# Optimization experiments

Hardware: AMD Instinct MI355X
Metric: run time of the kernel (lower is better)

## Reference

```python
import jax, jax.numpy as jnp
import numpy as np

N_HEAD = 16

def setup_inputs() -> dict:
    key = jax.random.key(0)
    k1, k2, k3, k4, k5 = jax.random.split(key, 5)
    B, T, C = 8, 2048, 1024
    hs = C // N_HEAD  # 64
    return {
        "ids": jax.random.normal(k1, (B, T, C), dtype=jnp.float32),
        "qkv_w": jax.random.normal(k2, (3 * hs, C), dtype=jnp.float32) * (C ** -0.5),
        "qkv_b": jax.random.normal(k3, (3 * hs,), dtype=jnp.float32) * 0.02,
        "proj_w": jax.random.normal(k4, (C, C), dtype=jnp.float32) * (C ** -0.5),
        "proj_b": jax.random.normal(k5, (C,), dtype=jnp.float32) * 0.02,
    }

def reference(ids, qkv_w, qkv_b, proj_w, proj_b):
    B, T, C = ids.shape
    hs = qkv_w.shape[0] // 3  # head_size
    # All heads share the same qkv Linear (input is replicated per-head in the
    # original), so compute one head and tile at the end.
    qkv = ids @ qkv_w.T + qkv_b                      # [B,T,3*hs]
    q, k, v = jnp.split(qkv, 3, axis=-1)             # each [B,T,hs]
    wei = jnp.einsum('btd,bsd->bts', q, k)           # [B,T,T]
    tril = jnp.tril(jnp.ones((T, T), dtype=bool))
    wei = jnp.where(tril, wei, jnp.float32(0.0))     # causal mask (no softmax)
    out_h = jnp.einsum('bts,bsd->btd', wei, v)       # [B,T,hs]
    out = jnp.tile(out_h, (1, 1, N_HEAD))            # identical heads concatenated
    return out @ proj_w.T + proj_b                   # [B,T,C]
```

## Files before the change

### kernel.cpp

```cpp
#include <hip/hip_runtime.h>
#include <hip/hip_bf16.h>

#define Bsz 8
#define Tsz 2048
#define Csz 1024
#define HSsz 64
#define NQ 192

typedef __attribute__((ext_vector_type(8))) short short8v;
typedef __attribute__((ext_vector_type(4))) float f32x4;
typedef unsigned short ushortT;
typedef unsigned int uintT;

__device__ __forceinline__ unsigned int f2bf(float f) {
    union { float f; unsigned int u; } v; v.f = f;
    return (v.u + 0x7fffu + ((v.u >> 16) & 1u)) >> 16;
}

__device__ __forceinline__ unsigned int pk2bf(float lo, float hi) {
    union { __hip_bfloat162 h2; unsigned int u; } cv;
    cv.h2 = __float22bfloat162_rn(float2{lo, hi});
    return cv.u;
}

__device__ __forceinline__ void glds16(const float* g, float* l) {
    __builtin_amdgcn_global_load_lds(
        (const __attribute__((address_space(1))) unsigned int*)(g),
        (__attribute__((address_space(3))) unsigned int*)(l),
        16, 0, 0);
}

__global__ __launch_bounds__(256) void k_prep(const float* __restrict__ qw,
                                              const float* __restrict__ pw,
                                              ushortT* __restrict__ wB,
                                              ushortT* __restrict__ w2a) {
    const int blk = blockIdx.x;
    if (blk < 96) {
        int idx = blk * 256 + threadIdx.x;
        int l = idx & 63;
        int ksjt = idx >> 6;
        int jt = ksjt % 12, ks = ksjt / 12;
        int j = jt * 16 + (l & 15);
        int k = ks * 32 + (l >> 4) * 8;
        const float* src = &qw[j * Csz + k];
        float4 a = *(const float4*)src;
        float4 b = *(const float4*)(src + 4);
        uint4 o;
        o.x = f2bf(a.x) | (f2bf(a.y) << 16);
        o.y = f2bf(a.z) | (f2bf(a.w) << 16);
        o.z = f2bf(b.x) | (f2bf(b.y) << 16);
        o.w = f2bf(b.z) | (f2bf(b.w) << 16);
        *(uint4*)&wB[(size_t)idx * 8] = o;
    } else {
        int idx = (blk - 96) * 256 + threadIdx.x;
        int l = idx & 63;
        int rest = idx >> 6;
        int m = rest & 63, ks = rest >> 6;
        int c = m * 16 + (l & 15);
        int d0 = ks * 32 + (l >> 4) * 8;
        float s0 = 0, s1 = 0, s2 = 0, s3 = 0, s4 = 0, s5 = 0, s6 = 0, s7 = 0;
#pragma unroll
        for (int hh = 0; hh < 16; ++hh) {
            const float* p = &pw[c * Csz + hh * HSsz + d0];
            float4 x = *(const float4*)p;
            float4 y = *(const float4*)(p + 4);
            s0 += x.x; s1 += x.y; s2 += x.z; s3 += x.w;
            s4 += y.x; s5 += y.y; s6 += y.z; s7 += y.w;
        }
        uint4 o;
        o.x = f2bf(s0) | (f2bf(s1) << 16);
        o.y = f2bf(s2) | (f2bf(s3) << 16);
        o.z = f2bf(s4) | (f2bf(s5) << 16);
        o.w = f2bf(s6) | (f2bf(s7) << 16);
        *(uint4*)&w2a[(size_t)idx * 8] = o;
    }
}

__global__ __launch_bounds__(512, 4) void k_qkv_mfma(const float* __restrict__ ids,
                                                     const ushortT* __restrict__ wB,
                                                     const float* __restrict__ bias,
                                                     ushortT* __restrict__ Qf,
                                                     ushortT* __restrict__ Kf,
                                                     ushortT* __restrict__ Vf) {
    __shared__ float sAf[2][4096];
    uintT* Lqk = (uintT*)&sAf[0][0];
    uintT* Lv  = Lqk + 32 * 68;

    const int tid = threadIdx.x;
    const int wv  = tid >> 6;
    const int l   = tid & 63;
    const int wm  = wv >> 2;
    const int wn  = wv & 3;
    const int lg  = l >> 4, ll = l & 15;

    const int row0 = blockIdx.x * 32;

    const int r0 = 4 * wv + (l >> 5);
    const int r2 = r0 + 2;
    const int g  = l & 31;
    const float* s0 = ids + (size_t)(row0 + r0) * Csz + ((g ^ (r0 & 7)) << 2);
    const float* s1 = ids + (size_t)(row0 + r2) * Csz + ((g ^ (r2 & 7)) << 2);

    const int afrow = wm * 16 + ll;
    const int e = ll & 7;

    f32x4 acc[3];
    acc[0] = acc[1] = acc[2] = (f32x4){0.f, 0.f, 0.f, 0.f};

    const ushortT* bbase_p = wB + ((size_t)(wn * 3) * 64 + l) * 8;

    glds16(s0, &sAf[0][wv * 512]);
    glds16(s1, &sAf[0][wv * 512 + 256]);

    for (int c = 0; c < 8; ++c) {
        __syncthreads();
        if (c < 7) {
            glds16(s0 + (c + 1) * 128, &sAf[(c + 1) & 1][wv * 512]);
            glds16(s1 + (c + 1) * 128, &sAf[(c + 1) & 1][wv * 512 + 256]);
        }
        const float* bufp = &sAf[c & 1][0];
#pragma unroll
        for (int kk = 0; kk < 4; ++kk) {
            const ushortT* bp = bbase_p + (size_t)(4 * c + kk) * 6144;
            short8v b0 = *(const short8v*)(bp);
            short8v b1 = *(const short8v*)(bp + 512);
            short8v b2 = *(const short8v*)(bp + 1024);

            const int G0 = kk * 8 + lg * 2;
            float4 a0 = *(const float4*)&bufp[afrow * 128 + ((G0 ^ e) << 2)];
            float4 a1 = *(const float4*)&bufp[afrow * 128 + (((G0 + 1) ^ e) << 2)];

            union { short8v s; unsigned int u[4]; } af;
            af.u[0] = pk2bf(a0.x, a0.y); af.u[1] = pk2bf(a0.z, a0.w);
            af.u[2] = pk2bf(a1.x, a1.y); af.u[3] = pk2bf(a1.z, a1.w);

            acc[0] = __builtin_amdgcn_mfma_f32_16x16x32_bf16(af.s, b0, acc[0], 0, 0, 0);
            acc[1] = __builtin_amdgcn_mfma_f32_16x16x32_bf16(af.s, b1, acc[1], 0, 0, 0);
            acc[2] = __builtin_amdgcn_mfma_f32_16x16x32_bf16(af.s, b2, acc[2], 0, 0, 0);
        }
    }
    __syncthreads();

    const int crow_l = wm * 16 + lg * 4;
    ushortT* L16 = (ushortT*)Lqk;
#pragma unroll
    for (int n = 0; n < 3; ++n) {
        const int jb = wn * 3 + n;
        const int j  = jb * 16 + ll;
        const float bj = bias[j];
        float v0 = acc[n][0] + bj, v1 = acc[n][1] + bj;
        float v2 = acc[n][2] + bj, v3 = acc[n][3] + bj;
        if (jb < 8) {
            ushortT* p = &L16[crow_l * 136 + j];
            p[0]   = (ushortT)f2bf(v0);
            p[136] = (ushortT)f2bf(v1);
            p[272] = (ushortT)f2bf(v2);
            p[408] = (ushortT)f2bf(v3);
        } else {
            uintT* p = &Lv[(j - 128) * 20 + (crow_l >> 1)];
            p[0] = pk2bf(v0, v1);
            p[1] = pk2bf(v2, v3);
        }
    }
    __syncthreads();

    const int l2 = tid & 63, ll2 = l2 & 15, lg2 = l2 >> 4;
    if (tid < 256) {
        const int ks = (tid >> 6) & 1, m = tid >> 7;
        uint4 q = *(const uint4*)&Lqk[(m * 16 + ll2) * 68 + ks * 16 + lg2 * 4];
        *(uint4*)&Qf[(((size_t)(row0 >> 4) + m) * 2 + ks) * 512 + l2 * 8] = q;
        const int n = tid >> 6;
        uint4 v = *(const uint4*)&Lv[(n * 16 + ll2) * 20 + lg2 * 4];
        const int bb = row0 >> 11, s32 = (row0 >> 5) & 63;
        *(uint4*)&Vf[((((size_t)bb * 64 + s32) * 4 + n) * 64 + l2) * 8] = v;
    } else {
        const int ks = (tid >> 6) & 1, m = (tid >> 7) & 1;
        uint4 k = *(const uint4*)&Lqk[(m * 16 + ll2) * 68 + 32 + ks * 16 + lg2 * 4];
        *(uint4*)&Kf[(((size_t)(row0 >> 4) + m) * 2 + ks) * 512 + l2 * 8] = k;
    }
}

__global__ __launch_bounds__(256, 3) void k_attn_mfma(const ushortT* __restrict__ Qf,
                                                      const ushortT* __restrict__ Kf,
                                                      const ushortT* __restrict__ Vf,
                                                      ushortT* __restrict__ hf) {
    __shared__ uintT su[4 * 2 * 16 * 36];
    __shared__ float s_o[4][32 * 68];

    const int tid = threadIdx.x;
    const int w  = tid >> 6;
    const int l  = tid & 63;
    const int lg = l >> 4;
    const int ll = l & 15;

    const int u = blockIdx.x;
    const int b = u & 7;
    const int si = 63 - (u >> 3);

    const int nT  = (si >> 1) + 1;
    const int qn  = nT >> 2, rem = nT & 3;
    const int t0  = w * qn + (w < rem ? w : rem);
    const int cnt = qn + (w < rem ? 1 : 0);

    const int gq = b * 128 + si * 2;

    short8v qf[2][2];
#pragma unroll
    for (int mt = 0; mt < 2; ++mt)
#pragma unroll
        for (int ks = 0; ks < 2; ++ks)
            qf[mt][ks] = *(const short8v*)&Qf[(((size_t)gq + mt) * 2 + ks) * 512 + l * 8];

    f32x4 oacc[2][4];
#pragma unroll
    for (int mt = 0; mt < 2; ++mt)
#pragma unroll
        for (int n = 0; n < 4; ++n) oacc[mt][n] = (f32x4){0.f, 0.f, 0.f, 0.f};

    for (int tile = t0; tile < t0 + cnt; ++tile) {
        const int gs = b * 128 + tile * 4;
        short8v kf[4][2];
#pragma unroll
        for (int ms = 0; ms < 4; ++ms) {
            const ushortT* kp = &Kf[(((size_t)gs + ms) * 2) * 512 + l * 8];
            kf[ms][0] = *(const short8v*)kp;
            kf[ms][1] = *(const short8v*)(kp + 512);
        }
        f32x4 sacc[4][2];
#pragma unroll
        for (int ms = 0; ms < 4; ++ms)
#pragma unroll
            for (int mt = 0; mt < 2; ++mt) sacc[ms][mt] = (f32x4){0.f, 0.f, 0.f, 0.f};
#pragma unroll
        for (int ms = 0; ms < 4; ++ms)
#pragma unroll
            for (int mt = 0; mt < 2; ++mt) {
                sacc[ms][mt] = __builtin_amdgcn_mfma_f32_16x16x32_bf16(kf[ms][0], qf[mt][0], sacc[ms][mt], 0, 0, 0);
                sacc[ms][mt] = __builtin_amdgcn_mfma_f32_16x16x32_bf16(kf[ms][1], qf[mt][1], sacc[ms][mt], 0, 0, 0);
            }
        if (tile == nT - 1) {
#pragma unroll
            for (int ms = 0; ms < 4; ++ms)
#pragma unroll
                for (int mt = 0; mt < 2; ++mt) {
                    const int tg = si * 32 + mt * 16 + ll;
#pragma unroll
                    for (int rr2 = 0; rr2 < 4; ++rr2) {
                        int sg = tile * 64 + ms * 16 + 4 * lg + rr2;
                        if (sg > tg) sacc[ms][mt][rr2] = 0.f;
                    }
                }
        }
#pragma unroll
        for (int mt = 0; mt < 2; ++mt)
#pragma unroll
            for (int ms = 0; ms < 4; ++ms) {
                uint2 pk;
                pk.x = pk2bf(sacc[ms][mt][0], sacc[ms][mt][1]);
                pk.y = pk2bf(sacc[ms][mt][2], sacc[ms][mt][3]);
                *(uint2*)&su[((w * 2 + mt) * 16 + ll) * 36 + ms * 8 + 2 * lg] = pk;
            }
        union { uint4 u4; short8v s; } pa[2][2];
#pragma unroll
        for (int mt = 0; mt < 2; ++mt)
#pragma unroll
            for (int h = 0; h < 2; ++h)
                pa[mt][h].u4 = *(const uint4*)&su[((w * 2 + mt) * 16 + ll) * 36 + h * 16 + lg * 4];

        const int gv = b * 64 + tile * 2;
        short8v vf[2][4];
#pragma unroll
        for (int h = 0; h < 2; ++h)
#pragma unroll
            for (int n = 0; n < 4; ++n)
                vf[h][n] = *(const short8v*)&Vf[((((size_t)gv + h) * 4 + n) * 64 + l) * 8];
#pragma unroll
        for (int mt = 0; mt < 2; ++mt)
#pragma unroll
            for (int n = 0; n < 4; ++n) {
                oacc[mt][n] = __builtin_amdgcn_mfma_f32_16x16x32_bf16(pa[mt][0].s, vf[0][n], oacc[mt][n], 0, 0, 0);
                oacc[mt][n] = __builtin_amdgcn_mfma_f32_16x16x32_bf16(pa[mt][1].s, vf[1][n], oacc[mt][n], 0, 0, 0);
            }
    }

#pragma unroll
    for (int mt = 0; mt < 2; ++mt)
#pragma unroll
        for (int n = 0; n < 4; ++n)
#pragma unroll
            for (int rr2 = 0; rr2 < 4; ++rr2)
                s_o[w][(mt * 16 + 4 * lg + rr2) * 68 + 16 * n + ll] = oacc[mt][n][rr2];
    __syncthreads();

    const int l2 = tid & 63, ll2 = l2 & 15, lg2 = l2 >> 4;
    const int ks = (tid >> 6) & 1, mt = tid >> 7;
    const int t = mt * 16 + ll2, dd = ks * 32 + lg2 * 8;
    float4 A = {0, 0, 0, 0}, B2 = {0, 0, 0, 0};
#pragma unroll
    for (int w2 = 0; w2 < 4; ++w2) {
        const float4 x = *(const float4*)&s_o[w2][t * 68 + dd];
        const float4 y = *(const float4*)&s_o[w2][t * 68 + dd + 4];
        A.x += x.x; A.y += x.y; A.z += x.z; A.w += x.w;
        B2.x += y.x; B2.y += y.y; B2.z += y.z; B2.w += y.w;
    }
    uint4 o;
    o.x = pk2bf(A.x, A.y);  o.y = pk2bf(A.z, A.w);
    o.z = pk2bf(B2.x, B2.y); o.w = pk2bf(B2.z, B2.w);
    *(uint4*)&hf[(((size_t)(b * 128 + si * 2) + mt) * 2 + ks) * 512 + l2 * 8] = o;
}

__global__ __launch_bounds__(256) void k_proj_mfma(const ushortT* __restrict__ hf,
                                                   const ushortT* __restrict__ w2a,
                                                   const float* __restrict__ pb,
                                                   float* __restrict__ out) {
    const int tid = threadIdx.x;
    const int w = tid >> 6, l = tid & 63;
    const size_t M0 = (size_t)blockIdx.x * 2;

    short8v hA0 = *(const short8v*)&hf[(M0 * 2 + 0) * 512 + l * 8];
    short8v hA1 = *(const short8v*)&hf[(M0 * 2 + 1) * 512 + l * 8];
    short8v hB0 = *(const short8v*)&hf[((M0 + 1) * 2 + 0) * 512 + l * 8];
    short8v hB1 = *(const short8v*)&hf[((M0 + 1) * 2 + 1) * 512 + l * 8];

    const int row = (l >> 4) * 4;
    const int tcol = l & 15;
    const size_t outA = (M0 * 16 + tcol) * Csz;
    const size_t outB = ((M0 + 1) * 16 + tcol) * Csz;

#pragma unroll 2
    for (int m = w * 16; m < w * 16 + 16; ++m) {
        const ushortT* ap = w2a + (size_t)(m * 64 + l) * 8;
        short8v a0 = *(const short8v*)ap;
        short8v a1 = *(const short8v*)(ap + 32768);
        const int c0 = m * 16 + row;
        const float4 pv = *(const float4*)&pb[c0];

        f32x4 accA = (f32x4){0.f, 0.f, 0.f, 0.f};
        accA = __builtin_amdgcn_mfma_f32_16x16x32_bf16(a0, hA0, accA, 0, 0, 0);
        accA = __builtin_amdgcn_mfma_f32_16x16x32_bf16(a1, hA1, accA, 0, 0, 0);
        f32x4 accB = (f32x4){0.f, 0.f, 0.f, 0.f};
        accB = __builtin_amdgcn_mfma_f32_16x16x32_bf16(a0, hB0, accB, 0, 0, 0);
        accB = __builtin_amdgcn_mfma_f32_16x16x32_bf16(a1, hB1, accB, 0, 0, 0);

        float4 oA, oB;
        oA.x = accA[0] + pv.x; oA.y = accA[1] + pv.y;
        oA.z = accA[2] + pv.z; oA.w = accA[3] + pv.w;
        oB.x = accB[0] + pv.x; oB.y = accB[1] + pv.y;
        oB.z = accB[2] + pv.z; oB.w = accB[3] + pv.w;
        *(float4*)&out[outA + c0] = oA;
        *(float4*)&out[outB + c0] = oB;
    }
}

extern "C" void kernel_launch(void* const* d_in, const int* in_sizes, int n_in,
                              void* d_out, int out_size, void* d_ws, size_t ws_size,
                              hipStream_t stream) {
    const float* ids    = (const float*)d_in[0];
    const float* qkv_w  = (const float*)d_in[1];
    const float* qkv_b  = (const float*)d_in[2];
    const float* proj_w = (const float*)d_in[3];
    const float* proj_b = (const float*)d_in[4];
    float* out = (float*)d_out;

    ushortT* Qf  = (ushortT*)d_ws;
    ushortT* Kf  = Qf + 16384 * HSsz;
    ushortT* Vf  = Kf + 16384 * HSsz;
    ushortT* hf  = Vf + 16384 * HSsz;
    ushortT* wB  = hf + 16384 * HSsz;
    ushortT* w2a = wB + 196608;

    hipLaunchKernelGGL(k_prep,      dim3(128), dim3(256), 0, stream, qkv_w, proj_w, wB, w2a);
    hipLaunchKernelGGL(k_qkv_mfma,  dim3(512), dim3(512), 0, stream, ids, wB, qkv_b, Qf, Kf, Vf);
    hipLaunchKernelGGL(k_attn_mfma, dim3(512), dim3(256), 0, stream, Qf, Kf, Vf, hf);
    hipLaunchKernelGGL(k_proj_mfma, dim3(512), dim3(256), 0, stream, hf, w2a, proj_b, out);
}
```

Measured before the change: 59.95 us.

## Use linear-attention prefix K^T V sums to replace off-chunk attention tiles

Because there is no softmax, the causal product can be split by associativity. A new kernel computes prefix sums of K^T V per 256-row chunk (stored in bf16), and the attention kernel then handles only the at most 4 diagonal-chunk tiles directly, adding Q·M for everything earlier. This removes the quadratic off-diagonal QK^T/PV work. In exchange it adds an extra Ktf transpose write, an extra launch, a serial prefix loop in k_kvsum (64 blocks, up to 56 iterations), and bf16 rounding of the accumulated prefix matrix.

```diff
diff --git a/kernel.cpp b/kernel.cpp
--- a/kernel.cpp
+++ b/kernel.cpp
@@ -81,10 +81,12 @@
                                                      const float* __restrict__ bias,
                                                      ushortT* __restrict__ Qf,
                                                      ushortT* __restrict__ Kf,
-                                                     ushortT* __restrict__ Vf) {
+                                                     ushortT* __restrict__ Vf,
+                                                     ushortT* __restrict__ Ktf) {
     __shared__ float sAf[2][4096];
     uintT* Lqk = (uintT*)&sAf[0][0];
     uintT* Lv  = Lqk + 32 * 68;
+    uintT* Lkt = Lv + 64 * 20;
 
     const int tid = threadIdx.x;
     const int wv  = tid >> 6;
@@ -156,6 +158,11 @@
             p[136] = (ushortT)f2bf(v1);
             p[272] = (ushortT)f2bf(v2);
             p[408] = (ushortT)f2bf(v3);
+            if (jb >= 4) {
+                uintT* pk = &Lkt[(j - 64) * 20 + (crow_l >> 1)];
+                pk[0] = pk2bf(v0, v1);
+                pk[1] = pk2bf(v2, v3);
+            }
         } else {
             uintT* p = &Lv[(j - 128) * 20 + (crow_l >> 1)];
             p[0] = pk2bf(v0, v1);
@@ -165,24 +172,71 @@
     __syncthreads();
 
     const int l2 = tid & 63, ll2 = l2 & 15, lg2 = l2 >> 4;
+    const int bb = row0 >> 11, s32 = (row0 >> 5) & 63;
     if (tid < 256) {
         const int ks = (tid >> 6) & 1, m = tid >> 7;
         uint4 q = *(const uint4*)&Lqk[(m * 16 + ll2) * 68 + ks * 16 + lg2 * 4];
         *(uint4*)&Qf[(((size_t)(row0 >> 4) + m) * 2 + ks) * 512 + l2 * 8] = q;
         const int n = tid >> 6;
         uint4 v = *(const uint4*)&Lv[(n * 16 + ll2) * 20 + lg2 * 4];
-        const int bb = row0 >> 11, s32 = (row0 >> 5) & 63;
         *(uint4*)&Vf[((((size_t)bb * 64 + s32) * 4 + n) * 64 + l2) * 8] = v;
     } else {
         const int ks = (tid >> 6) & 1, m = (tid >> 7) & 1;
         uint4 k = *(const uint4*)&Lqk[(m * 16 + ll2) * 68 + 32 + ks * 16 + lg2 * 4];
         *(uint4*)&Kf[(((size_t)(row0 >> 4) + m) * 2 + ks) * 512 + l2 * 8] = k;
+        const int n = (tid >> 6) & 3;
+        uint4 kt = *(const uint4*)&Lkt[(n * 16 + ll2) * 20 + lg2 * 4];
+        *(uint4*)&Ktf[((((size_t)bb * 64 + s32) * 4 + n) * 64 + l2) * 8] = kt;
+    }
+}
+
+__global__ __launch_bounds__(256) void k_kvsum(const ushortT* __restrict__ Ktf,
+                                               const ushortT* __restrict__ Vf,
+                                               ushortT* __restrict__ Mf) {
+    __shared__ float Msum[64 * 68];
+    const int tid = threadIdx.x;
+    const int w = tid >> 6, l = tid & 63;
+    const int lg = l >> 4, ll = l & 15;
+    const int b = blockIdx.x >> 3, cc = blockIdx.x & 7;
+
+    f32x4 acc[4];
+#pragma unroll
+    for (int m = 0; m < 4; ++m) acc[m] = (f32x4){0.f, 0.f, 0.f, 0.f};
+
+    const int ns = cc * 8;
+    for (int s32 = 0; s32 < ns; ++s32) {
+        const size_t base = (size_t)(b * 64 + s32) * 4;
+        short8v vfr = *(const short8v*)&Vf[((base + w) * 64 + l) * 8];
+#pragma unroll
+        for (int m = 0; m < 4; ++m) {
+            short8v kfr = *(const short8v*)&Ktf[((base + m) * 64 + l) * 8];
+            acc[m] = __builtin_amdgcn_mfma_f32_16x16x32_bf16(kfr, vfr, acc[m], 0, 0, 0);
+        }
+    }
+#pragma unroll
+    for (int m = 0; m < 4; ++m)
+#pragma unroll
+        for (int r = 0; r < 4; ++r)
+            Msum[(m * 16 + 4 * lg + r) * 68 + w * 16 + ll] = acc[m][r];
+    __syncthreads();
+
+#pragma unroll
+    for (int ks = 0; ks < 2; ++ks) {
+        float v[8];
+#pragma unroll
+        for (int b8 = 0; b8 < 8; ++b8)
+            v[b8] = Msum[(ks * 32 + lg * 8 + b8) * 68 + w * 16 + ll];
+        uint4 o;
+        o.x = pk2bf(v[0], v[1]); o.y = pk2bf(v[2], v[3]);
+        o.z = pk2bf(v[4], v[5]); o.w = pk2bf(v[6], v[7]);
+        *(uint4*)&Mf[(((size_t)(b * 8 + cc)) * 8 + ks * 4 + w) * 512 + l * 8] = o;
     }
 }
 
 __global__ __launch_bounds__(256, 3) void k_attn_mfma(const ushortT* __restrict__ Qf,
                                                       const ushortT* __restrict__ Kf,
                                                       const ushortT* __restrict__ Vf,
+                                                      const ushortT* __restrict__ Mf,
                                                       ushortT* __restrict__ hf) {
     __shared__ uintT su[4 * 2 * 16 * 36];
     __shared__ float s_o[4][32 * 68];
@@ -197,10 +251,10 @@
     const int b = u & 7;
     const int si = 63 - (u >> 3);
 
-    const int nT  = (si >> 1) + 1;
-    const int qn  = nT >> 2, rem = nT & 3;
-    const int t0  = w * qn + (w < rem ? w : rem);
-    const int cnt = qn + (w < rem ? 1 : 0);
+    const int cc    = si >> 3;
+    const int nT    = (si >> 1) + 1;
+    const int tbase = cc << 2;
+    const int cnt   = nT - tbase;
 
     const int gq = b * 128 + si * 2;
 
@@ -217,7 +271,8 @@
 #pragma unroll
         for (int n = 0; n < 4; ++n) oacc[mt][n] = (f32x4){0.f, 0.f, 0.f, 0.f};
 
-    for (int tile = t0; tile < t0 + cnt; ++tile) {
+    if (w < cnt) {
+        const int tile = tbase + w;
         const int gs = b * 128 + tile * 4;
         short8v kf[4][2];
 #pragma unroll
@@ -283,13 +338,28 @@
             }
     }
 
+    f32x4 inter[2];
+    inter[0] = inter[1] = (f32x4){0.f, 0.f, 0.f, 0.f};
+    {
+        const size_t mbase = (((size_t)(b * 8 + cc)) * 8 + w) * 512 + l * 8;
+        short8v mf0 = *(const short8v*)&Mf[mbase];
+        short8v mf1 = *(const short8v*)&Mf[mbase + 4 * 512];
+#pragma unroll
+        for (int mt = 0; mt < 2; ++mt) {
+            inter[mt] = __builtin_amdgcn_mfma_f32_16x16x32_bf16(qf[mt][0], mf0, inter[mt], 0, 0, 0);
+            inter[mt] = __builtin_amdgcn_mfma_f32_16x16x32_bf16(qf[mt][1], mf1, inter[mt], 0, 0, 0);
+        }
+    }
+
 #pragma unroll
     for (int mt = 0; mt < 2; ++mt)
 #pragma unroll
         for (int n = 0; n < 4; ++n)
 #pragma unroll
-            for (int rr2 = 0; rr2 < 4; ++rr2)
-                s_o[w][(mt * 16 + 4 * lg + rr2) * 68 + 16 * n + ll] = oacc[mt][n][rr2];
+            for (int rr2 = 0; rr2 < 4; ++rr2) {
+                float v = oacc[mt][n][rr2] + (n == w ? inter[mt][rr2] : 0.f);
+                s_o[w][(mt * 16 + 4 * lg + rr2) * 68 + 16 * n + ll] = v;
+            }
     __syncthreads();
 
     const int l2 = tid & 63, ll2 = l2 & 15, lg2 = l2 >> 4;
@@ -365,12 +435,15 @@
     ushortT* Qf  = (ushortT*)d_ws;
     ushortT* Kf  = Qf + 16384 * HSsz;
     ushortT* Vf  = Kf + 16384 * HSsz;
-    ushortT* hf  = Vf + 16384 * HSsz;
+    ushortT* Ktf = Vf + 16384 * HSsz;
+    ushortT* hf  = Ktf + 16384 * HSsz;
     ushortT* wB  = hf + 16384 * HSsz;
     ushortT* w2a = wB + 196608;
+    ushortT* Mf  = w2a + 65536;
 
     hipLaunchKernelGGL(k_prep,      dim3(128), dim3(256), 0, stream, qkv_w, proj_w, wB, w2a);
-    hipLaunchKernelGGL(k_qkv_mfma,  dim3(512), dim3(512), 0, stream, ids, wB, qkv_b, Qf, Kf, Vf);
-    hipLaunchKernelGGL(k_attn_mfma, dim3(512), dim3(256), 0, stream, Qf, Kf, Vf, hf);
+    hipLaunchKernelGGL(k_qkv_mfma,  dim3(512), dim3(512), 0, stream, ids, wB, qkv_b, Qf, Kf, Vf, Ktf);
+    hipLaunchKernelGGL(k_kvsum,     dim3(64),  dim3(256), 0, stream, Ktf, Vf, Mf);
+    hipLaunchKernelGGL(k_attn_mfma, dim3(512), dim3(256), 0, stream, Qf, Kf, Vf, Mf, hf);
     hipLaunchKernelGGL(k_proj_mfma, dim3(512), dim3(256), 0, stream, hf, w2a, proj_b, out);
 }
```

After: 73.85 us. 1.23x slower.
